# Kernel tuning notes

Hardware: AMD Instinct MI355X
Metric: run time of the kernel (lower is better)

## Reference

```python
import jax, jax.numpy as jnp
import numpy as np

HIDDEN = 2048
N_HEADS = 16
N_KV = 4
HEAD_DIM = 128
THETA = 500000.0
FREQ_ALLOC = 20  # t section; h = w = (HEAD_DIM//2 - 20)//2 = 22
T = 2048


def setup_inputs() -> dict:
    key = jax.random.key(0)
    k1, k2, k3, k4 = jax.random.split(key, 4)
    positions = jax.random.randint(k1, (3, T), 0, 1024, dtype=jnp.int32)
    hidden_states = jax.random.normal(k2, (T, HIDDEN), dtype=jnp.float32)
    w_qkv = jax.random.normal(k3, (HIDDEN, (N_HEADS + 2 * N_KV) * HEAD_DIM), dtype=jnp.float32) * 0.02
    w_o = jax.random.normal(k4, (N_HEADS * HEAD_DIM, HIDDEN), dtype=jnp.float32) * 0.02
    return {"positions": positions, "hidden_states": hidden_states, "w_qkv": w_qkv, "w_o": w_o}


def _mrope_cos_sin(positions):
    # standard rope table evaluated at positions: cos/sin each [3, T, HEAD_DIM//2]
    inv_freq = 1.0 / (THETA ** (jnp.arange(0, HEAD_DIM, 2, dtype=jnp.float32) / HEAD_DIM))
    freqs = positions.astype(jnp.float32)[..., None] * inv_freq
    cos, sin = jnp.cos(freqs), jnp.sin(freqs)
    sh = (HEAD_DIM // 2 - FREQ_ALLOC) // 2  # 22

    def section(c):
        c_t = c[0, :, -FREQ_ALLOC:]          # time dims from t-positions
        c_h = c[1, :, 0:2 * sh:2]            # even low-freq dims from h-positions
        c_w = c[2, :, 1:2 * sh:2]            # odd low-freq dims from w-positions
        c_hw = jnp.stack([c_h, c_w], axis=-1).reshape(c_h.shape[0], 2 * sh)
        return jnp.concatenate([c_hw, c_t], axis=-1)  # [T, HEAD_DIM//2]

    return section(cos), section(sin)


def _rotate_interleaved(x, cos, sin):
    # is_neox_style=False: even/odd interleaved rotation. x: [T, H, HEAD_DIM]
    x1, x2 = x[..., 0::2], x[..., 1::2]
    c, s = cos[:, None, :], sin[:, None, :]
    o1 = x1 * c - x2 * s
    o2 = x2 * c + x1 * s
    return jnp.stack([o1, o2], axis=-1).reshape(x.shape)


def reference(positions, hidden_states, w_qkv, w_o):
    q_size = N_HEADS * HEAD_DIM
    kv_size = N_KV * HEAD_DIM
    qkv = hidden_states @ w_qkv  # [T, 3072]
    q = qkv[:, :q_size].reshape(T, N_HEADS, HEAD_DIM)
    k = qkv[:, q_size:q_size + kv_size].reshape(T, N_KV, HEAD_DIM)
    v = qkv[:, q_size + kv_size:].reshape(T, N_KV, HEAD_DIM)

    cos, sin = _mrope_cos_sin(positions)
    q = _rotate_interleaved(q, cos, sin)
    k = _rotate_interleaved(k, cos, sin)

    # GQA causal attention
    rep = N_HEADS // N_KV
    kr = jnp.repeat(k, rep, axis=1)  # [T, N_HEADS, D]
    vr = jnp.repeat(v, rep, axis=1)
    scale = HEAD_DIM ** -0.5
    scores = jnp.einsum('qhd,khd->hqk', q, kr) * scale
    causal = jnp.tril(jnp.ones((T, T), dtype=bool))
    scores = jnp.where(causal[None], scores, jnp.finfo(scores.dtype).min)
    attn = jax.nn.softmax(scores, axis=-1)
    out = jnp.einsum('hqk,khd->qhd', attn, vr).reshape(T, N_HEADS * HEAD_DIM)
    return out @ w_o
```

## Files before the change

### kernel.cpp

```cpp
#include <hip/hip_runtime.h>
#include <math.h>

#define T 2048
#define HIDDEN 2048
#define NH 16
#define NKV 4
#define HD 128
#define QKV_N 3072
#define Q_SIZE 2048
#define KV_SIZE 512

typedef __attribute__((ext_vector_type(8))) short short8;
typedef __attribute__((ext_vector_type(4))) short short4v;
typedef __attribute__((ext_vector_type(4))) float floatx4;
typedef __attribute__((ext_vector_type(16))) float floatx16;

#define VMCNT(N) asm volatile("s_waitcnt vmcnt(" #N ")" ::: "memory")
#define LGKMCNT0 asm volatile("s_waitcnt lgkmcnt(0)" ::: "memory")
#define BARRIER_RAW()                          \
    do {                                       \
        __builtin_amdgcn_s_barrier();          \
        asm volatile("" ::: "memory");         \
    } while (0)

__device__ __forceinline__ unsigned short f2bf(float f) {
    union { float f; unsigned int u; } v; v.f = f;
    unsigned int u = v.u;
    u += 0x7fffu + ((u >> 16) & 1u);
    return (unsigned short)(u >> 16);
}

__device__ __forceinline__ void gload_lds16(const unsigned short* g, unsigned short* l) {
    __builtin_amdgcn_global_load_lds((const __attribute__((address_space(1))) unsigned int*)g,
                                     (__attribute__((address_space(3))) unsigned int*)l, 16, 0, 0);
}

__global__ __launch_bounds__(256) void prep_misc(const float* __restrict__ hidden,
                                                 const float* __restrict__ w_qkv,
                                                 const float* __restrict__ w_o,
                                                 const int* __restrict__ positions,
                                                 unsigned short* __restrict__ hb,
                                                 unsigned short* __restrict__ wqt,
                                                 unsigned short* __restrict__ wot,
                                                 float* __restrict__ cosT,
                                                 float* __restrict__ sinT) {
    __shared__ float tile[32][33];
    const int b = blockIdx.x;
    const int tid = threadIdx.x;
    const int tx = tid & 31, ty = tid >> 5;

    if (b < 4096) {
        int i = (b * 256 + tid) * 4;
        float4 v = *(const float4*)(hidden + i);
        hb[i]     = f2bf(v.x);
        hb[i + 1] = f2bf(v.y);
        hb[i + 2] = f2bf(v.z);
        hb[i + 3] = f2bf(v.w);
    } else if (b < 10240) {
        int idx = b - 4096;
        int c0 = (idx % 96) * 32, r0 = (idx / 96) * 32;
#pragma unroll
        for (int i = 0; i < 4; ++i)
            tile[ty + i * 8][tx] = w_qkv[(long)(r0 + ty + i * 8) * QKV_N + c0 + tx];
        __syncthreads();
#pragma unroll
        for (int i = 0; i < 4; ++i)
            wqt[(long)(c0 + ty + i * 8) * HIDDEN + r0 + tx] = f2bf(tile[tx][ty + i * 8]);
    } else if (b < 14336) {
        int idx = b - 10240;
        int c0 = (idx % 64) * 32, r0 = (idx / 64) * 32;
#pragma unroll
        for (int i = 0; i < 4; ++i)
            tile[ty + i * 8][tx] = w_o[(long)(r0 + ty + i * 8) * HIDDEN + c0 + tx];
        __syncthreads();
#pragma unroll
        for (int i = 0; i < 4; ++i)
            wot[(long)(c0 + ty + i * 8) * HIDDEN + r0 + tx] = f2bf(tile[tx][ty + i * 8]);
    } else {
        int idx = b - 14336;
        int t = idx * 4 + (tid >> 6);
        int j = tid & 63;
        int row = (j >= 44) ? 0 : ((j & 1) ? 2 : 1);
        int pos = positions[row * T + t];
        float invf = exp2f((float)j * -0.29580571f);
        float ang = (float)pos * invf;
        cosT[t * 64 + j] = cosf(ang);
        sinT[t * 64 + j] = sinf(ang);
    }
}

__global__ __launch_bounds__(256) void gemm_qkv(const unsigned short* __restrict__ A,
                                                const unsigned short* __restrict__ B,
                                                const float* __restrict__ cosT,
                                                const float* __restrict__ sinT,
                                                unsigned short* __restrict__ qb,
                                                unsigned short* __restrict__ kb,
                                                unsigned short* __restrict__ vt) {
    __shared__ __align__(16) unsigned short Ls[3][320 * 64];
    const int tid = threadIdx.x;
    const int wv = tid >> 6;
    const int lane = tid & 63;
    const int l31 = lane & 31;
    const int hi = lane >> 5;
    const int wr = wv >> 1, wc = wv & 1;
    const int by = blockIdx.x;
    const int bx = blockIdx.y;
    const unsigned short* Ab = A + (long)(bx * 128) * HIDDEN;
    const unsigned short* Bb = B + (long)(by * 192) * HIDDEN;

    floatx16 acc[2][3];
#pragma unroll
    for (int i = 0; i < 2; ++i)
#pragma unroll
        for (int j = 0; j < 3; ++j) acc[i][j] = (floatx16)0.0f;

#define QKV_STAGE(bufidx, k0)                                                          \
    do {                                                                               \
        unsigned short* lb_ = &Ls[bufidx][0];                                          \
        _Pragma("unroll") for (int qq_ = 0; qq_ < 10; ++qq_) {                         \
            int q_ = qq_ * 4 + wv;                                                     \
            int s_ = q_ * 64 + lane;                                                   \
            int r_ = s_ >> 3;                                                          \
            int c_ = (s_ & 7) ^ (r_ & 7);                                              \
            const unsigned short* src_ = (qq_ < 4)                                     \
                ? (Ab + (long)r_ * HIDDEN + (k0) + c_ * 8)                             \
                : (Bb + (long)(r_ - 128) * HIDDEN + (k0) + c_ * 8);                    \
            gload_lds16(src_, lb_ + q_ * 512);                                         \
        }                                                                              \
    } while (0)

    QKV_STAGE(0, 0);
    QKV_STAGE(1, 64);
    int cur = 0;
    const int arow0 = wr * 64 + l31;
    const int brow0 = 128 + wc * 96 + l31;
#pragma unroll 1
    for (int t = 0; t < 32; ++t) {
        if (t < 31) VMCNT(10); else VMCNT(0);
        BARRIER_RAW();
        if (t + 2 < 32) {
            int nb = cur + 2; if (nb >= 3) nb -= 3;
            QKV_STAGE(nb, (t + 2) * 64);
        }
        const unsigned short* lb = &Ls[cur][0];
#pragma unroll
        for (int kk = 0; kk < 4; ++kk) {
            const int ck = kk * 2 + hi;
            short8 a[2], b[3];
#pragma unroll
            for (int i = 0; i < 2; ++i) {
                const int row = arow0 + i * 32;
                a[i] = *(const short8*)&lb[row * 64 + ((ck ^ (row & 7)) << 3)];
            }
#pragma unroll
            for (int j = 0; j < 3; ++j) {
                const int row = brow0 + j * 32;
                b[j] = *(const short8*)&lb[row * 64 + ((ck ^ (row & 7)) << 3)];
            }
#pragma unroll
            for (int i = 0; i < 2; ++i)
#pragma unroll
                for (int j = 0; j < 3; ++j)
                    acc[i][j] = __builtin_amdgcn_mfma_f32_32x32x16_bf16(a[i], b[j], acc[i][j], 0, 0, 0);
        }
        LGKMCNT0;
        cur = (cur == 2) ? 0 : cur + 1;
    }
#undef QKV_STAGE

    const float qscale = 0.08838834764831845f;
#pragma unroll
    for (int i = 0; i < 2; ++i) {
#pragma unroll
        for (int j = 0; j < 3; ++j) {
            const int colbase = by * 192 + wc * 96 + j * 32;
            const int col = colbase + l31;
            const int trow0 = bx * 128 + wr * 64 + i * 32 + 4 * hi;
            if (colbase < Q_SIZE + KV_SIZE) {
                const float sgn = (col & 1) ? 1.f : -1.f;
                const int j2 = (col & 127) >> 1;
#pragma unroll
                for (int h = 0; h < 4; ++h) {
#pragma unroll
                    for (int r = 0; r < 4; ++r) {
                        const int tt = trow0 + 8 * h + r;
                        float val = acc[i][j][h * 4 + r];
                        float prt = __shfl_xor(val, 1);
                        float o = val * cosT[tt * 64 + j2] + sgn * prt * sinT[tt * 64 + j2];
                        if (colbase < Q_SIZE)
                            qb[(long)tt * Q_SIZE + col] = f2bf(o * qscale);
                        else
                            kb[(long)tt * KV_SIZE + (col - Q_SIZE)] = f2bf(o);
                    }
                }
            } else {
                const int vcol = col - (Q_SIZE + KV_SIZE);
                const int g = vcol >> 7, d = vcol & 127;
#pragma unroll
                for (int h = 0; h < 4; ++h) {
                    const int t0 = trow0 + 8 * h;
                    unsigned short o4[4];
#pragma unroll
                    for (int r = 0; r < 4; ++r) o4[r] = f2bf(acc[i][j][h * 4 + r]);
                    *(short4v*)&vt[((long)g * HD + d) * T + t0] = *(short4v*)o4;
                }
            }
        }
    }
}

__global__ __launch_bounds__(256) void gemm_out(const unsigned short* __restrict__ A,
                                                const unsigned short* __restrict__ B,
                                                float* __restrict__ C,
                                                int K, int ldc) {
    __shared__ __align__(16) unsigned short Ls[3][256 * 64];
    const int tid = threadIdx.x;
    const int wv = tid >> 6;
    const int lane = tid & 63;
    const int l31 = lane & 31;
    const int hi = lane >> 5;
    const int wr = wv >> 1, wc = wv & 1;
    const int by = blockIdx.x;
    const int bx = blockIdx.y;
    const unsigned short* Ab = A + (long)(bx * 128) * K;
    const unsigned short* Bb = B + (long)(by * 128) * K;

    floatx16 acc[2][2];
#pragma unroll
    for (int i = 0; i < 2; ++i)
#pragma unroll
        for (int j = 0; j < 2; ++j) acc[i][j] = (floatx16)0.0f;

#define OUT_STAGE(bufidx, k0)                                                          \
    do {                                                                               \
        unsigned short* lb_ = &Ls[bufidx][0];                                          \
        _Pragma("unroll") for (int qq_ = 0; qq_ < 8; ++qq_) {                          \
            int q_ = qq_ * 4 + wv;                                                     \
            int s_ = q_ * 64 + lane;                                                   \
            int r_ = s_ >> 3;                                                          \
            int c_ = (s_ & 7) ^ (r_ & 7);                                              \
            const unsigned short* src_ = (q_ < 16)                                     \
                ? (Ab + (long)r_ * K + (k0) + c_ * 8)                                  \
                : (Bb + (long)(r_ - 128) * K + (k0) + c_ * 8);                         \
            gload_lds16(src_, lb_ + q_ * 512);                                         \
        }                                                                              \
    } while (0)

    const int NT = K >> 6;
    OUT_STAGE(0, 0);
    OUT_STAGE(1, 64);
    int cur = 0;
    const int arow0 = wr * 64 + l31;
    const int brow0 = 128 + wc * 64 + l31;
#pragma unroll 1
    for (int t = 0; t < NT; ++t) {
        if (t < NT - 1) VMCNT(8); else VMCNT(0);
        BARRIER_RAW();
        if (t + 2 < NT) {
            int nb = cur + 2; if (nb >= 3) nb -= 3;
            OUT_STAGE(nb, (t + 2) * 64);
        }
        const unsigned short* lb = &Ls[cur][0];
#pragma unroll
        for (int kk = 0; kk < 4; ++kk) {
            const int ck = kk * 2 + hi;
            short8 a[2], b[2];
#pragma unroll
            for (int i = 0; i < 2; ++i) {
                const int row = arow0 + i * 32;
                a[i] = *(const short8*)&lb[row * 64 + ((ck ^ (row & 7)) << 3)];
            }
#pragma unroll
            for (int j = 0; j < 2; ++j) {
                const int row = brow0 + j * 32;
                b[j] = *(const short8*)&lb[row * 64 + ((ck ^ (row & 7)) << 3)];
            }
#pragma unroll
            for (int i = 0; i < 2; ++i)
#pragma unroll
                for (int j = 0; j < 2; ++j)
                    acc[i][j] = __builtin_amdgcn_mfma_f32_32x32x16_bf16(a[i], b[j], acc[i][j], 0, 0, 0);
        }
        LGKMCNT0;
        cur = (cur == 2) ? 0 : cur + 1;
    }
#undef OUT_STAGE

#pragma unroll
    for (int i = 0; i < 2; ++i)
#pragma unroll
        for (int j = 0; j < 2; ++j) {
            const long rbase = (long)(bx * 128 + wr * 64 + i * 32 + 4 * hi);
            const int cbase = by * 128 + wc * 64 + j * 32 + l31;
#pragma unroll
            for (int h = 0; h < 4; ++h)
#pragma unroll
                for (int r = 0; r < 4; ++r)
                    C[(rbase + 8 * h + r) * ldc + cbase] = acc[i][j][h * 4 + r];
        }
}

__global__ __launch_bounds__(256, 2) void flash_attn(const unsigned short* __restrict__ qb,
                                                     const unsigned short* __restrict__ kb,
                                                     const unsigned short* __restrict__ vt,
                                                     float* __restrict__ Opart,
                                                     float* __restrict__ MLpart) {
    __shared__ __align__(16) unsigned short Kbuf[2][64 * 128];
    __shared__ __align__(16) unsigned short Vbuf[128 * 64];
    __shared__ __align__(16) unsigned short Pls[4][32 * 72];

    const int tid = threadIdx.x;
    const int wv = tid >> 6;
    const int lane = tid & 63;
    const int m = lane & 15;
    const int qd = lane >> 4;

    const int bx = blockIdx.x;
    const int c_ = bx & 255;
    const int hi = bx >> 8;
    const int h = c_ >> 4;
    const int j_ = c_ & 15;
    const int qt = hi ? (j_ >> 1) : (15 - (j_ >> 1));
    const int half = j_ & 1;
    const int g = h >> 2;
    unsigned short* myP = Pls[wv];

    const int n0 = qt + 1;
    const int jt0 = half ? n0 : 0;
    const int jt1 = half ? 2 * qt + 2 : n0;
    const int q0 = qt * 128;

    short8 aq[2][4];
#pragma unroll
    for (int s = 0; s < 2; ++s)
#pragma unroll
        for (int kk = 0; kk < 4; ++kk)
            aq[s][kk] = *(const short8*)(qb + (long)(q0 + s * 64 + wv * 16 + m) * Q_SIZE +
                                         h * HD + kk * 32 + qd * 8);

    floatx4 acc_o[2][8];
#pragma unroll
    for (int s = 0; s < 2; ++s)
#pragma unroll
        for (int nb = 0; nb < 8; ++nb) acc_o[s][nb] = (floatx4){0.f, 0.f, 0.f, 0.f};
    float mrow[2] = {-1e30f, -1e30f};
    float lrow[2] = {0.f, 0.f};

#pragma unroll
    for (int i = 0; i < 4; ++i) {
        int s_ = i * 256 + tid;
        int r = s_ >> 4, c = (s_ & 15) ^ (r & 15);
        gload_lds16(kb + (long)(jt0 * 64 + r) * KV_SIZE + g * HD + c * 8,
                    &Kbuf[0][i * 2048 + wv * 512]);
    }
    int cur = 0;
    for (int jt = jt0; jt < jt1; ++jt) {
        VMCNT(0);
        BARRIER_RAW();

#pragma unroll
        for (int i = 0; i < 4; ++i) {
            int s_ = i * 256 + tid;
            int r = s_ >> 3, c = (s_ & 7) ^ (r & 7);
            gload_lds16(vt + ((long)g * HD + r) * T + jt * 64 + c * 8,
                        &Vbuf[i * 2048 + wv * 512]);
        }
        const bool pk = (jt + 1 < jt1);
        if (pk) {
#pragma unroll
            for (int i = 0; i < 4; ++i) {
                int s_ = i * 256 + tid;
                int r = s_ >> 4, c = (s_ & 15) ^ (r & 15);
                gload_lds16(kb + (long)((jt + 1) * 64 + r) * KV_SIZE + g * HD + c * 8,
                            &Kbuf[cur ^ 1][i * 2048 + wv * 512]);
            }
        }

        floatx4 acc_s[2][4];
#pragma unroll
        for (int s = 0; s < 2; ++s)
#pragma unroll
            for (int c = 0; c < 4; ++c) acc_s[s][c] = (floatx4){0.f, 0.f, 0.f, 0.f};
#pragma unroll
        for (int kk = 0; kk < 4; ++kk) {
#pragma unroll
            for (int c = 0; c < 4; ++c) {
                short8 ak = *(const short8*)&Kbuf[cur][(c * 16 + m) * 128 +
                                                       (((4 * kk + qd) ^ m) * 8)];
                acc_s[0][c] = __builtin_amdgcn_mfma_f32_16x16x32_bf16(ak, aq[0][kk], acc_s[0][c], 0, 0, 0);
                acc_s[1][c] = __builtin_amdgcn_mfma_f32_16x16x32_bf16(ak, aq[1][kk], acc_s[1][c], 0, 0, 0);
            }
        }

#pragma unroll
        for (int s = 0; s < 2; ++s) {
            const int dg = 2 * qt + s;
            if (jt >= dg) {
                const bool full = (jt > dg);
#pragma unroll
                for (int c = 0; c < 4; ++c)
#pragma unroll
                    for (int r = 0; r < 4; ++r)
                        if (full || (c * 16 + qd * 4 + r > wv * 16 + m)) acc_s[s][c][r] = -1e30f;
            }
            float mx = acc_s[s][0][0];
#pragma unroll
            for (int c = 0; c < 4; ++c)
#pragma unroll
                for (int r = 0; r < 4; ++r) mx = fmaxf(mx, acc_s[s][c][r]);
            mx = fmaxf(mx, __shfl_xor(mx, 16));
            mx = fmaxf(mx, __shfl_xor(mx, 32));
            float mnew = fmaxf(mrow[s], mx);
            float alpha = __expf(mrow[s] - mnew);
            mrow[s] = mnew;

            float pv[4][4];
            float lsum = 0.f;
#pragma unroll
            for (int c = 0; c < 4; ++c)
#pragma unroll
                for (int r = 0; r < 4; ++r) {
                    pv[c][r] = __expf(acc_s[s][c][r] - mnew);
                    lsum += pv[c][r];
                }
            lsum += __shfl_xor(lsum, 16);
            lsum += __shfl_xor(lsum, 32);
            lrow[s] = lrow[s] * alpha + lsum;
#pragma unroll
            for (int nb = 0; nb < 8; ++nb)
#pragma unroll
                for (int r = 0; r < 4; ++r) acc_o[s][nb][r] *= alpha;
#pragma unroll
            for (int c = 0; c < 4; ++c) {
                short4v pk2 = {(short)f2bf(pv[c][0]), (short)f2bf(pv[c][1]),
                               (short)f2bf(pv[c][2]), (short)f2bf(pv[c][3])};
                *(short4v*)&myP[(s * 16 + m) * 72 + c * 16 + qd * 4] = pk2;
            }
        }

        if (pk) VMCNT(4); else VMCNT(0);
        BARRIER_RAW();

#pragma unroll
        for (int kk = 0; kk < 2; ++kk) {
            short8 pa0 = *(const short8*)&myP[m * 72 + kk * 32 + qd * 8];
            short8 pa1 = *(const short8*)&myP[(16 + m) * 72 + kk * 32 + qd * 8];
#pragma unroll
            for (int nb = 0; nb < 8; ++nb) {
                short8 av = *(const short8*)&Vbuf[(nb * 16 + m) * 64 +
                                                  (((4 * kk + qd) ^ (m & 7)) * 8)];
                acc_o[0][nb] = __builtin_amdgcn_mfma_f32_16x16x32_bf16(av, pa0, acc_o[0][nb], 0, 0, 0);
                acc_o[1][nb] = __builtin_amdgcn_mfma_f32_16x16x32_bf16(av, pa1, acc_o[1][nb], 0, 0, 0);
            }
        }
        LGKMCNT0;
        cur ^= 1;
    }

    const int unit = (h * 16 + qt) * 2 + half;
#pragma unroll
    for (int s = 0; s < 2; ++s) {
        const long rb = (long)unit * 128 + s * 64 + wv * 16 + m;
#pragma unroll
        for (int nb = 0; nb < 8; ++nb)
            *(floatx4*)&Opart[rb * 128 + nb * 16 + qd * 4] = acc_o[s][nb];
        if (qd == 0) {
            MLpart[rb * 2]     = mrow[s];
            MLpart[rb * 2 + 1] = lrow[s];
        }
    }
}

__global__ __launch_bounds__(256) void attn_combine(const float* __restrict__ Opart,
                                                    const float* __restrict__ MLpart,
                                                    unsigned short* __restrict__ ab) {
    const int tid = threadIdx.x;
    const int q = blockIdx.x * 16 + (tid >> 4);
    const int h = blockIdx.y;
    const int d0 = (tid & 15) * 8;
    const int qt = q >> 7, lr = q & 127;
    const long r0 = ((long)(h * 16 + qt) * 2) * 128 + lr;
    const long r1 = r0 + 128;
    float m0 = MLpart[r0 * 2], l0 = MLpart[r0 * 2 + 1];
    float m1 = MLpart[r1 * 2], l1 = MLpart[r1 * 2 + 1];
    float M = fmaxf(m0, m1);
    float a0 = __expf(m0 - M), a1 = __expf(m1 - M);
    float inv = 1.f / (l0 * a0 + l1 * a1);
    const float* O0 = Opart + r0 * 128 + d0;
    const float* O1 = Opart + r1 * 128 + d0;
    unsigned short outv[8];
#pragma unroll
    for (int j = 0; j < 8; j += 4) {
        float4 x0 = *(const float4*)(O0 + j);
        float4 x1 = *(const float4*)(O1 + j);
        outv[j]     = f2bf((x0.x * a0 + x1.x * a1) * inv);
        outv[j + 1] = f2bf((x0.y * a0 + x1.y * a1) * inv);
        outv[j + 2] = f2bf((x0.z * a0 + x1.z * a1) * inv);
        outv[j + 3] = f2bf((x0.w * a0 + x1.w * a1) * inv);
    }
    *(short8*)&ab[(long)q * Q_SIZE + h * HD + d0] = *(short8*)outv;
}

extern "C" void kernel_launch(void* const* d_in, const int* in_sizes, int n_in,
                              void* d_out, int out_size, void* d_ws, size_t ws_size,
                              hipStream_t stream) {
    const int* positions = (const int*)d_in[0];
    const float* hidden  = (const float*)d_in[1];
    const float* w_qkv   = (const float*)d_in[2];
    const float* w_o     = (const float*)d_in[3];
    float* out = (float*)d_out;

    char* p = (char*)d_ws;
    auto alloc = [&](size_t bytes) { char* r = p; p += (bytes + 255) & ~(size_t)255; return r; };
    float* cosT = (float*)alloc((size_t)T * 64 * 4);
    float* sinT = (float*)alloc((size_t)T * 64 * 4);
    unsigned short* hb  = (unsigned short*)alloc((size_t)T * HIDDEN * 2);
    unsigned short* wqt = (unsigned short*)alloc((size_t)QKV_N * HIDDEN * 2);
    unsigned short* wot = (unsigned short*)alloc((size_t)HIDDEN * HIDDEN * 2);
    unsigned short* qb  = (unsigned short*)alloc((size_t)T * Q_SIZE * 2);
    unsigned short* kb  = (unsigned short*)alloc((size_t)T * KV_SIZE * 2);
    unsigned short* vt  = (unsigned short*)alloc((size_t)T * KV_SIZE * 2);
    unsigned short* ab  = (unsigned short*)alloc((size_t)T * Q_SIZE * 2);
    float* Opart  = (float*)alloc((size_t)512 * 128 * 128 * 4);
    float* MLpart = (float*)alloc((size_t)512 * 128 * 2 * 4);

    prep_misc<<<dim3(14848), 256, 0, stream>>>(hidden, w_qkv, w_o, positions,
                                               hb, wqt, wot, cosT, sinT);
    gemm_qkv<<<dim3(QKV_N / 192, T / 128), 256, 0, stream>>>(hb, wqt, cosT, sinT, qb, kb, vt);
    flash_attn<<<dim3(512), 256, 0, stream>>>(qb, kb, vt, Opart, MLpart);
    attn_combine<<<dim3(T / 16, NH), 256, 0, stream>>>(Opart, MLpart, ab);
    gemm_out<<<dim3(HIDDEN / 128, T / 128), 256, 0, stream>>>(ab, wot, out, Q_SIZE, HIDDEN);
}
```

Measured before the change: 223.4 us.

## Retile QKV GEMM to 64x128 blocks with 16x16x32 MFMA

Changes the QKV projection GEMM from 128x192 tiles using 32x32 MFMA to 64x128 tiles using 16x16x32 MFMA, with separate A/B LDS buffers and a transposed grid (t-blocks along x). The launch count rises from 256 to 768 blocks, which is meant to improve occupancy and load balance across CUs. Each block tile now aligns with a single head group, so the RoPE/V-transpose epilogue branches per block. The cost is lower arithmetic intensity per tile and more global reloads of A and B.

```diff
diff --git a/kernel.cpp b/kernel.cpp
--- a/kernel.cpp
+++ b/kernel.cpp
@@ -96,116 +96,101 @@
                                                 unsigned short* __restrict__ qb,
                                                 unsigned short* __restrict__ kb,
                                                 unsigned short* __restrict__ vt) {
-    __shared__ __align__(16) unsigned short Ls[3][320 * 64];
+    __shared__ __align__(16) unsigned short As[3][64 * 64];
+    __shared__ __align__(16) unsigned short Bs[3][128 * 64];
+    const int K = HIDDEN;
     const int tid = threadIdx.x;
     const int wv = tid >> 6;
     const int lane = tid & 63;
-    const int l31 = lane & 31;
-    const int hi = lane >> 5;
-    const int wr = wv >> 1, wc = wv & 1;
-    const int by = blockIdx.x;
-    const int bx = blockIdx.y;
-    const unsigned short* Ab = A + (long)(bx * 128) * HIDDEN;
-    const unsigned short* Bb = B + (long)(by * 192) * HIDDEN;
-
-    floatx16 acc[2][3];
-#pragma unroll
-    for (int i = 0; i < 2; ++i)
-#pragma unroll
-        for (int j = 0; j < 3; ++j) acc[i][j] = (floatx16)0.0f;
-
-#define QKV_STAGE(bufidx, k0)                                                          \
-    do {                                                                               \
-        unsigned short* lb_ = &Ls[bufidx][0];                                          \
-        _Pragma("unroll") for (int qq_ = 0; qq_ < 10; ++qq_) {                         \
-            int q_ = qq_ * 4 + wv;                                                     \
-            int s_ = q_ * 64 + lane;                                                   \
-            int r_ = s_ >> 3;                                                          \
-            int c_ = (s_ & 7) ^ (r_ & 7);                                              \
-            const unsigned short* src_ = (qq_ < 4)                                     \
-                ? (Ab + (long)r_ * HIDDEN + (k0) + c_ * 8)                             \
-                : (Bb + (long)(r_ - 128) * HIDDEN + (k0) + c_ * 8);                    \
-            gload_lds16(src_, lb_ + q_ * 512);                                         \
-        }                                                                              \
+    const int m = lane & 15, qd = lane >> 4;
+    const unsigned short* Ab = A + (long)(blockIdx.x * 64) * K;
+    const unsigned short* Bb = B + (long)(blockIdx.y * 128) * K;
+
+    floatx4 acc[4][2];
+#pragma unroll
+    for (int i = 0; i < 4; ++i)
+#pragma unroll
+        for (int j = 0; j < 2; ++j) acc[i][j] = (floatx4){0.f, 0.f, 0.f, 0.f};
+
+#define QKV_STAGE(buf, k0)                                                                   \
+    do {                                                                                     \
+        _Pragma("unroll") for (int i_ = 0; i_ < 2; ++i_) {                                   \
+            int s_ = i_ * 256 + tid, r_ = s_ >> 3, c_ = (s_ & 7) ^ (r_ & 7);                 \
+            gload_lds16(Ab + (long)r_ * K + (k0) + c_ * 8, &As[buf][i_ * 2048 + wv * 512]);  \
+        }                                                                                    \
+        _Pragma("unroll") for (int i_ = 0; i_ < 4; ++i_) {                                   \
+            int s_ = i_ * 256 + tid, r_ = s_ >> 3, c_ = (s_ & 7) ^ (r_ & 7);                 \
+            gload_lds16(Bb + (long)r_ * K + (k0) + c_ * 8, &Bs[buf][i_ * 2048 + wv * 512]);  \
+        }                                                                                    \
     } while (0)
 
     QKV_STAGE(0, 0);
     QKV_STAGE(1, 64);
     int cur = 0;
-    const int arow0 = wr * 64 + l31;
-    const int brow0 = 128 + wc * 96 + l31;
 #pragma unroll 1
     for (int t = 0; t < 32; ++t) {
-        if (t < 31) VMCNT(10); else VMCNT(0);
+        if (t < 31) VMCNT(6); else VMCNT(0);
         BARRIER_RAW();
         if (t + 2 < 32) {
             int nb = cur + 2; if (nb >= 3) nb -= 3;
             QKV_STAGE(nb, (t + 2) * 64);
         }
-        const unsigned short* lb = &Ls[cur][0];
-#pragma unroll
-        for (int kk = 0; kk < 4; ++kk) {
-            const int ck = kk * 2 + hi;
-            short8 a[2], b[3];
-#pragma unroll
-            for (int i = 0; i < 2; ++i) {
-                const int row = arow0 + i * 32;
-                a[i] = *(const short8*)&lb[row * 64 + ((ck ^ (row & 7)) << 3)];
-            }
-#pragma unroll
-            for (int j = 0; j < 3; ++j) {
-                const int row = brow0 + j * 32;
-                b[j] = *(const short8*)&lb[row * 64 + ((ck ^ (row & 7)) << 3)];
-            }
-#pragma unroll
-            for (int i = 0; i < 2; ++i)
-#pragma unroll
-                for (int j = 0; j < 3; ++j)
-                    acc[i][j] = __builtin_amdgcn_mfma_f32_32x32x16_bf16(a[i], b[j], acc[i][j], 0, 0, 0);
+#pragma unroll
+        for (int kk = 0; kk < 2; ++kk) {
+            const int rch = ((kk * 4 + qd) ^ (m & 7)) * 8;
+            short8 a[4], b[2];
+#pragma unroll
+            for (int i = 0; i < 4; ++i) a[i] = *(const short8*)&As[cur][(i * 16 + m) * 64 + rch];
+#pragma unroll
+            for (int j = 0; j < 2; ++j) b[j] = *(const short8*)&Bs[cur][(wv * 32 + j * 16 + m) * 64 + rch];
+#pragma unroll
+            for (int i = 0; i < 4; ++i)
+#pragma unroll
+                for (int j = 0; j < 2; ++j)
+                    acc[i][j] = __builtin_amdgcn_mfma_f32_16x16x32_bf16(a[i], b[j], acc[i][j], 0, 0, 0);
         }
         LGKMCNT0;
         cur = (cur == 2) ? 0 : cur + 1;
     }
 #undef QKV_STAGE
 
-    const float qscale = 0.08838834764831845f;
-#pragma unroll
-    for (int i = 0; i < 2; ++i) {
-#pragma unroll
-        for (int j = 0; j < 3; ++j) {
-            const int colbase = by * 192 + wc * 96 + j * 32;
-            const int col = colbase + l31;
-            const int trow0 = bx * 128 + wr * 64 + i * 32 + 4 * hi;
-            if (colbase < Q_SIZE + KV_SIZE) {
-                const float sgn = (col & 1) ? 1.f : -1.f;
-                const int j2 = (col & 127) >> 1;
-#pragma unroll
-                for (int h = 0; h < 4; ++h) {
-#pragma unroll
-                    for (int r = 0; r < 4; ++r) {
-                        const int tt = trow0 + 8 * h + r;
-                        float val = acc[i][j][h * 4 + r];
-                        float prt = __shfl_xor(val, 1);
-                        float o = val * cosT[tt * 64 + j2] + sgn * prt * sinT[tt * 64 + j2];
-                        if (colbase < Q_SIZE)
-                            qb[(long)tt * Q_SIZE + col] = f2bf(o * qscale);
-                        else
-                            kb[(long)tt * KV_SIZE + (col - Q_SIZE)] = f2bf(o);
-                    }
+    const int by = blockIdx.y;
+    if (by < 20) {
+        const float sgn = (m & 1) ? 1.f : -1.f;
+        const float qscale = 0.08838834764831845f;
+#pragma unroll
+        for (int i = 0; i < 4; ++i) {
+#pragma unroll
+            for (int r = 0; r < 4; ++r) {
+                const int t = blockIdx.x * 64 + i * 16 + qd * 4 + r;
+                const float* ct = cosT + t * 64;
+                const float* st = sinT + t * 64;
+#pragma unroll
+                for (int j = 0; j < 2; ++j) {
+                    const int cq = wv * 32 + j * 16 + m;
+                    const int j2 = cq >> 1;
+                    float val = acc[i][j][r];
+                    float prt = __shfl_xor(val, 1);
+                    float o = val * ct[j2] + sgn * prt * st[j2];
+                    const int col = by * 128 + cq;
+                    if (by < 16) qb[(long)t * Q_SIZE + col] = f2bf(o * qscale);
+                    else         kb[(long)t * KV_SIZE + (col - 2048)] = f2bf(o);
                 }
-            } else {
-                const int vcol = col - (Q_SIZE + KV_SIZE);
-                const int g = vcol >> 7, d = vcol & 127;
-#pragma unroll
-                for (int h = 0; h < 4; ++h) {
-                    const int t0 = trow0 + 8 * h;
-                    unsigned short o4[4];
-#pragma unroll
-                    for (int r = 0; r < 4; ++r) o4[r] = f2bf(acc[i][j][h * 4 + r]);
-                    *(short4v*)&vt[((long)g * HD + d) * T + t0] = *(short4v*)o4;
-                }
-            }
-        }
+            }
+        }
+    } else {
+        const int g = by - 20;
+#pragma unroll
+        for (int i = 0; i < 4; ++i)
+#pragma unroll
+            for (int j = 0; j < 2; ++j) {
+                const int d = wv * 32 + j * 16 + m;
+                const int t0 = blockIdx.x * 64 + i * 16 + qd * 4;
+                unsigned short o4[4];
+#pragma unroll
+                for (int r = 0; r < 4; ++r) o4[r] = f2bf(acc[i][j][r]);
+                *(short4v*)&vt[((long)g * HD + d) * T + t0] = *(short4v*)o4;
+            }
     }
 }
 
@@ -526,7 +511,7 @@
 
     prep_misc<<<dim3(14848), 256, 0, stream>>>(hidden, w_qkv, w_o, positions,
                                                hb, wqt, wot, cosT, sinT);
-    gemm_qkv<<<dim3(QKV_N / 192, T / 128), 256, 0, stream>>>(hb, wqt, cosT, sinT, qb, kb, vt);
+    gemm_qkv<<<dim3(T / 64, QKV_N / 128), 256, 0, stream>>>(hb, wqt, cosT, sinT, qb, kb, vt);
     flash_attn<<<dim3(512), 256, 0, stream>>>(qb, kb, vt, Opart, MLpart);
     attn_combine<<<dim3(T / 16, NH), 256, 0, stream>>>(Opart, MLpart, ab);
     gemm_out<<<dim3(HIDDEN / 128, T / 128), 256, 0, stream>>>(ab, wot, out, Q_SIZE, HIDDEN);
```

New measurement: 238.8 us. 6.9% more time.
